# Performance work log

Hardware: AMD Instinct MI355X
Metric: run time of the kernel (lower is better)

The kernel has to match this reference:

```python
import jax, jax.numpy as jnp
import numpy as np

B, W, C = 128, 64, 48
NUM_CHARS, E, H, HM, CTX, CTXM, OUT = 256, 64, 128, 128, 128, 128, 8


def _gru(x, lens, Wih, Whh, bih, bhh):
    """Masked unidirectional GRU. x: [N,T,D], lens: [N]. Outputs zero at t>=len
    (matching pad_packed_sequence), state frozen past len."""
    N, T, _ = x.shape
    Hd = Whh.shape[1]
    xg = jnp.einsum('ntd,gd->ntg', x, Wih) + bih  # [N,T,3H] precomputed input gates

    def step(h, inp):
        xg_t, t = inp
        hg = h @ Whh.T + bhh
        xr, xz, xn = jnp.split(xg_t, 3, axis=-1)
        hr, hz, hn = jnp.split(hg, 3, axis=-1)
        r = jax.nn.sigmoid(xr + hr)
        z = jax.nn.sigmoid(xz + hz)
        n = jnp.tanh(xn + r * hn)
        hnew = (1 - z) * n + z * h
        valid = (t < lens)[:, None]
        h2 = jnp.where(valid, hnew, h)
        out = jnp.where(valid, hnew, jnp.zeros_like(hnew))
        return h2, out

    h0 = jnp.zeros((N, Hd), x.dtype)
    _, outs = jax.lax.scan(step, h0, (xg.transpose(1, 0, 2), jnp.arange(T)))
    return outs.transpose(1, 0, 2)  # [N,T,H]


def _rev(x, lens):
    """Reverse each sequence within its valid length; pad positions unchanged."""
    T = x.shape[1]
    t = jnp.arange(T)[None, :]
    idx = jnp.where(t < lens[:, None], lens[:, None] - 1 - t, t)
    return jnp.take_along_axis(x, idx[:, :, None], axis=1)


def _bigru(x, lens, Wf, Uf, bif, bhf, Wb, Ub, bib, bhb):
    of = _gru(x, lens, Wf, Uf, bif, bhf)
    ob = _rev(_gru(_rev(x, lens), lens, Wb, Ub, bib, bhb), lens)
    return jnp.concatenate([of, ob], axis=-1)


def _attn_pool(out, Wp, bp, ctx):
    # out: [N,T,K]; softmax over ALL T positions (pads have out=0, faithful to source)
    proj = jnp.tanh(jnp.einsum('ntk,ck->ntc', out, Wp) + bp)
    att = jax.nn.softmax(proj @ ctx, axis=1)  # [N,T]
    return jnp.einsum('nt,ntk->nk', att, out)


def setup_inputs():
    key = jax.random.key(0)
    ks = iter(jax.random.split(key, 40))
    nrm = lambda shape: jax.random.normal(next(ks), shape, jnp.float32) * 0.1
    chars = jax.random.randint(next(ks), (B, W, C), 0, NUM_CHARS, dtype=jnp.int32)
    lens = jax.random.randint(next(ks), (B, W), 1, C + 1, dtype=jnp.int32)
    inp = dict(chars=chars, lens=lens, emb=nrm((NUM_CHARS, E)))
    for p, din, h in [('c', E, H), ('m', 2 * H, HM)]:
        for d in ('f', 'b'):
            inp[p + 'Wih_' + d] = nrm((3 * h, din))
            inp[p + 'Whh_' + d] = nrm((3 * h, h))
            inp[p + 'bih_' + d] = nrm((3 * h,))
            inp[p + 'bhh_' + d] = nrm((3 * h,))
    inp.update(wWp=nrm((CTX, 2 * H)), wbp=nrm((CTX,)), wctx=nrm((CTX,)),
               pWp=nrm((CTXM, 2 * HM)), pbp=nrm((CTXM,)), pctx=nrm((CTXM,)),
               Wout=nrm((OUT, 2 * HM)), bout=nrm((OUT,)))
    return inp


def reference(chars, lens, emb,
              cWih_f, cWhh_f, cbih_f, cbhh_f, cWih_b, cWhh_b, cbih_b, cbhh_b,
              mWih_f, mWhh_f, mbih_f, mbhh_f, mWih_b, mWhh_b, mbih_b, mbhh_b,
              wWp, wbp, wctx, pWp, pbp, pctx, Wout, bout):
    Bb, Ww, Cc = chars.shape
    x = emb[chars.reshape(Bb * Ww, Cc)]        # [B*W, C, E]
    l = lens.reshape(Bb * Ww)
    char_out = _bigru(x, l, cWih_f, cWhh_f, cbih_f, cbhh_f,
                      cWih_b, cWhh_b, cbih_b, cbhh_b)  # [B*W, C, 2H]
    words = _attn_pool(char_out, wWp, wbp, wctx).reshape(Bb, Ww, -1)  # [B, W, 2H]
    lw = jnp.full((Bb,), Ww, dtype=lens.dtype)
    msg_out = _bigru(words, lw, mWih_f, mWhh_f, mbih_f, mbhh_f,
                     mWih_b, mWhh_b, mbih_b, mbhh_b)  # [B, W, 2HM]
    messages = _attn_pool(msg_out, pWp, pbp, pctx)     # [B, 2HM]
    outputs = messages @ Wout.T + bout                 # [B, OUT]
    return outputs, messages
```

## Files before the change

### kernel.cpp

```cpp
#include <hip/hip_runtime.h>
#include <stdint.h>
#include <stddef.h>

#define NCH   256
#define EDIM  64
#define HDIM  128
#define G3    384
#define BATCH 128
#define WRD   64
#define CLEN  48
#define NW    8192
#define OUTD  8

#define LOG2E 1.44269504088896f

#define C_EMB     0
#define C_CWIH_F  16384
#define C_CWHH_F  40960
#define C_CBIH_F  90112
#define C_CBHH_F  90496
#define C_CWIH_B  90880
#define C_CWHH_B  115456
#define C_CBIH_B  164608
#define C_CBHH_B  164992
#define C_MWIH_F  165376
#define C_MWHH_F  263680
#define C_MBIH_F  312832
#define C_MBHH_F  313600
#define C_MWIH_B  314368
#define C_MWHH_B  412672
#define C_MBIH_B  461824
#define C_MBHH_B  462592
#define C_WWP     463360
#define C_WBP     496128
#define C_WCTX    496256
#define C_PWP     496384
#define C_PBP     529152
#define C_PCTX    529280
#define C_WOUT    529408
#define C_BOUT    531456
#define C_TOTAL   531464

#define OFF_FLAG    0u
#define OFF_CANON   1024u
#define OFF_WPFRAG  (4u*1024u*1024u)
#define OFF_PFRAG   (4u*1024u*1024u + 65536u)
#define OFF_MFRAG   (4u*1024u*1024u + 131072u)
#define OFF_BIASV   (4u*1024u*1024u + 524288u)
#define OFF_ORD     (4u*1024u*1024u + 532480u)
#define OFF_XGT4    5111808u
#define OFF_WORDS   35651584u
#define OFF_MSGOUT  47185920u
#define OFF_CHOUT   54525952u

typedef _Float16 h2v __attribute__((ext_vector_type(2)));
typedef _Float16 f16x8 __attribute__((ext_vector_type(8)));
typedef float f32x4 __attribute__((ext_vector_type(4)));

__device__ __forceinline__ float bf16_to_f32(unsigned short u){
  union{unsigned int i;float f;}v; v.i=((unsigned int)u)<<16; return v.f;
}
__device__ __forceinline__ unsigned short f32_to_bf16(float f){
  union{float f;unsigned int i;}v; v.f=f;
  unsigned int u=v.i; unsigned int r=(u + 0x7fffu + ((u>>16)&1u))>>16;
  return (unsigned short)r;
}
__device__ __forceinline__ uint32_t pack_h2(float x,float y){
  h2v h; h[0]=(_Float16)x; h[1]=(_Float16)y; uint32_t u; __builtin_memcpy(&u,&h,4); return u;
}
__device__ __forceinline__ unsigned short f32_to_h16u(float f){
  _Float16 h=(_Float16)f; unsigned short u; __builtin_memcpy(&u,&h,2); return u;
}
__device__ __forceinline__ float dot2(uint32_t a, uint32_t b, float c){
#if __has_builtin(__builtin_amdgcn_fdot2)
  h2v av,bv; __builtin_memcpy(&av,&a,4); __builtin_memcpy(&bv,&b,4);
  return __builtin_amdgcn_fdot2(av,bv,c,false);
#else
  h2v av,bv; __builtin_memcpy(&av,&a,4); __builtin_memcpy(&bv,&b,4);
  return c + (float)av[0]*(float)bv[0] + (float)av[1]*(float)bv[1];
#endif
}
__device__ __forceinline__ float exp2_fast(float x){
#if __has_builtin(__builtin_amdgcn_exp2f)
  return __builtin_amdgcn_exp2f(x);
#else
  return exp2f(x);
#endif
}
__device__ __forceinline__ float rcp_fast(float x){
#if __has_builtin(__builtin_amdgcn_rcpf)
  return __builtin_amdgcn_rcpf(x);
#else
  return 1.f/x;
#endif
}
__device__ __forceinline__ float sig2(float s){ return rcp_fast(1.f+exp2_fast(s)); }
__device__ __forceinline__ float tanh2(float u){ return fmaf(-2.f, rcp_fast(exp2_fast(u)+1.f), 1.f); }
__device__ __forceinline__ float wave_sum(float v){
  #pragma unroll
  for(int m=32;m>=1;m>>=1) v += __shfl_xor(v,m,64);
  return v;
}
__device__ __forceinline__ float wave_max(float v){
  #pragma unroll
  for(int m=32;m>=1;m>>=1) v = fmaxf(v,__shfl_xor(v,m,64));
  return v;
}
__device__ __forceinline__ f32x4 mfma16(f16x8 a, f16x8 b, f32x4 c){
  return __builtin_amdgcn_mfma_f32_16x16x32_f16(a, b, c, 0, 0, 0);
}

struct ConvArgs { const void* src[25]; int len[25]; int off[25]; };

__global__ void k_convert(ConvArgs a, int* __restrict__ flag, float* __restrict__ dst){
  const unsigned short* u=(const unsigned short*)a.src[0];
  int found=0;
  for(int i=threadIdx.x;i<2048;i+=256){ float v=bf16_to_f32(u[i]); if(fabsf(v)>8.f) found=1; }
  __shared__ int s;
  if(threadIdx.x==0) s=0;
  __syncthreads();
  if(found) atomicOr(&s,1);
  __syncthreads();
  int isf32=s;
  if(blockIdx.x==0 && threadIdx.x==0) *flag=isf32;
  int idx=blockIdx.x*256+threadIdx.x;
  #pragma unroll 1
  for(int i=0;i<25;i++){
    if(idx < a.len[i]){
      float v = isf32 ? ((const float*)a.src[i])[idx]
                      : bf16_to_f32(((const unsigned short*)a.src[i])[idx]);
      dst[a.off[i]+idx]=v;
      return;
    }
    idx -= a.len[i];
  }
}

__global__ void k_sort(const int* __restrict__ lensp, int* __restrict__ ord){
  __shared__ int hist[64];
  __shared__ int base[64];
  int tid=threadIdx.x;
  if(tid<64) hist[tid]=0;
  __syncthreads();
  for(int i=tid;i<NW;i+=256) atomicAdd(&hist[48-lensp[i]],1);
  __syncthreads();
  if(tid==0){ int s=0; for(int b=0;b<64;b++){ base[b]=s; s+=hist[b]; } }
  __syncthreads();
  for(int i=tid;i<NW;i+=256){
    int b=48-lensp[i];
    int pos=atomicAdd(&base[b],1);
    ord[pos]=i;
  }
}

__global__ void k_prep(const float* __restrict__ cw, unsigned short* __restrict__ wpfrag,
                       unsigned short* __restrict__ pfrag, unsigned short* __restrict__ mfrag,
                       float* __restrict__ biasv){
  int idx=blockIdx.x*256+threadIdx.x;
  if(idx<32768){
    int j=idx&7, lane=(idx>>3)&63, nt=(idx>>9)&7, ks=idx>>12;
    int nl=lane&15, q=lane>>4;
    float v = cw[C_WWP + (nt*16+nl)*256 + ks*32 + q*8 + j] * (2.f*LOG2E);
    wpfrag[idx]=f32_to_h16u(v);
  } else if(idx<65536){
    int i=idx-32768;
    int j=i&7, lane=(i>>3)&63, nt=(i>>9)&7, ks=i>>12;
    int nl=lane&15, q=lane>>4;
    float v = cw[C_PWP + (nt*16+nl)*256 + ks*32 + q*8 + j] * (2.f*LOG2E);
    pfrag[i]=f32_to_h16u(v);
  } else if(idx<262144){
    int i=idx-65536;
    int j=i&7, lane=(i>>3)&63, t2=i>>9;
    int nt=t2%48, ks=t2/48;
    int n=nt*16+(lane&15), k=ks*32+(lane>>4)*8+j;
    int gate = (n<G3)? n : n-G3;
    float sc = (gate<256)? -LOG2E : 2.f*LOG2E;
    float v = ((n<G3)? cw[C_MWIH_F + n*256 + k] : cw[C_MWIH_B + (n-G3)*256 + k]) * sc;
    mfrag[i]=f32_to_h16u(v);
  } else if(idx<262912){
    int i=idx-262144;
    int dir=i/384, g=i-384*(i/384);
    float b = cw[(dir?C_MBIH_B:C_MBIH_F)+g] + ((g<256)? cw[(dir?C_MBHH_B:C_MBHH_F)+g] : 0.f);
    biasv[i] = b * ((g<256)? -LOG2E : 2.f*LOG2E);
  } else if(idx==262912){
    float a=0.f;
    for(int c=0;c<128;c++) a += tanh2(cw[C_WBP+c]*(2.f*LOG2E))*cw[C_WCTX+c];
    biasv[768]=a;
  }
}

__global__ __launch_bounds__(512) void k_prepx(const float* __restrict__ cw,
                                               float4* __restrict__ xgt4){
  int tid=threadIdx.x;
  int w=tid>>6, L=tid&63, nl=L&15, q=L>>4;
  int mchunk=blockIdx.x, dir=blockIdx.y;
  const float* Wih=cw+(dir?C_CWIH_B:C_CWIH_F);
  const float* bih=cw+(dir?C_CBIH_B:C_CBIH_F);
  const float* bhh=cw+(dir?C_CBHH_B:C_CBHH_F);
  int c16=w*16+nl;

  f16x8 bw[3][2];
  #pragma unroll
  for(int i=0;i<3;i++){
    int n=(w+8*i)*16+nl;
    const float* wr=Wih + n*EDIM;
    #pragma unroll
    for(int ks=0;ks<2;ks++){
      const float4* p=(const float4*)(wr + ks*32 + q*8);
      float4 v0=p[0], v1=p[1];
      f16x8 f;
      f[0]=(_Float16)v0.x; f[1]=(_Float16)v0.y; f[2]=(_Float16)v0.z; f[3]=(_Float16)v0.w;
      f[4]=(_Float16)v1.x; f[5]=(_Float16)v1.y; f[6]=(_Float16)v1.z; f[7]=(_Float16)v1.w;
      bw[i][ks]=f;
    }
  }
  float br=bih[c16]+bhh[c16];
  float bz=bih[128+c16]+bhh[128+c16];
  float bn=bih[256+c16];

  #pragma unroll
  for(int mt=0;mt<2;mt++){
    int ch=mchunk*32+mt*16+nl;
    f32x4 ar={0,0,0,0}, az={0,0,0,0}, an={0,0,0,0};
    #pragma unroll
    for(int ks=0;ks<2;ks++){
      const float4* p=(const float4*)(cw + C_EMB + ch*EDIM + ks*32 + q*8);
      float4 v0=p[0], v1=p[1];
      f16x8 a;
      a[0]=(_Float16)v0.x; a[1]=(_Float16)v0.y; a[2]=(_Float16)v0.z; a[3]=(_Float16)v0.w;
      a[4]=(_Float16)v1.x; a[5]=(_Float16)v1.y; a[6]=(_Float16)v1.z; a[7]=(_Float16)v1.w;
      ar=mfma16(a,bw[0][ks],ar); az=mfma16(a,bw[1][ks],az); an=mfma16(a,bw[2][ks],an);
    }
    #pragma unroll
    for(int r=0;r<4;r++){
      int chr=mchunk*32+mt*16+q*4+r;
      xgt4[dir*32768 + chr*128 + c16] =
        make_float4((ar[r]+br)*(-LOG2E), (az[r]+bz)*(-LOG2E), (an[r]+bn)*(2.f*LOG2E), 0.f);
    }
  }
}

__global__ __launch_bounds__(512,4) void k_chargru(const int* __restrict__ chars,
    const int* __restrict__ lensp, const int* __restrict__ ord,
    const float* __restrict__ cw, const float4* __restrict__ xgt4,
    unsigned short* __restrict__ chout){
  int tid=threadIdx.x;
  int w=tid>>6, L=tid&63, nl=L&15, q=L>>4;
  int dir=blockIdx.y;
  int seq0=blockIdx.x*16;
  const float* Whh=cw+(dir?C_CWHH_B:C_CWHH_F);
  const float* bhh=cw+(dir?C_CBHH_B:C_CBHH_F);
  const float4* xg4 = xgt4 + (dir<<15);

  int c16=w*16+nl;
  f16x8 bh[3][4];
  const float wsc[3]={-LOG2E,-LOG2E,2.f*LOG2E};
  #pragma unroll
  for(int i=0;i<3;i++){
    int n=(w+8*i)*16+nl;
    const float* wr=Whh + n*HDIM;
    float sc=wsc[i];
    #pragma unroll
    for(int c=0;c<4;c++){
      const float4* p=(const float4*)(wr + c*32 + q*8);
      float4 v0=p[0], v1=p[1];
      f16x8 f;
      f[0]=(_Float16)(v0.x*sc); f[1]=(_Float16)(v0.y*sc); f[2]=(_Float16)(v0.z*sc); f[3]=(_Float16)(v0.w*sc);
      f[4]=(_Float16)(v1.x*sc); f[5]=(_Float16)(v1.y*sc); f[6]=(_Float16)(v1.z*sc); f[7]=(_Float16)(v1.w*sc);
      bh[i][c]=f;
    }
  }
  float bias_hn=bhh[256+c16]*(2.f*LOG2E);

  __shared__ int sord[16];
  __shared__ int cidT[CLEN][16];
  __shared__ int lenS[16];
  __shared__ __align__(16) _Float16 hbuf[2][16][136];

  if(tid<16) sord[tid]=ord[seq0+tid];
  __syncthreads();
  for(int i=tid;i<16*CLEN;i+=512){ int t=i>>4, s=i&15; cidT[t][s]=chars[sord[s]*CLEN+t]; }
  if(tid<16) lenS[tid]=lensp[sord[tid]];
  for(int i=tid;i<16*136/2;i+=512) ((uint32_t*)&hbuf[0][0][0])[i]=0u;
  __syncthreads();

  int maxlen=1;
  #pragma unroll 1
  for(int s=0;s<16;s++) maxlen=max(maxlen,lenS[s]);
  int lenq[4];
  #pragma unroll
  for(int r=0;r<4;r++) lenq[r]=lenS[q*4+r];
  int sw=tid>>5, aw=tid&31;
  int lenp=lenS[sw];
  int sq=sord[sw];

  float4 pf[4];
  {
    int t0 = dir ? maxlen-1 : 0;
    int4 c4=*(const int4*)&cidT[t0][q*4];
    pf[0]=xg4[c4.x*128+c16]; pf[1]=xg4[c4.y*128+c16];
    pf[2]=xg4[c4.z*128+c16]; pf[3]=xg4[c4.w*128+c16];
  }
  float hreg[4]={0.f,0.f,0.f,0.f};
  unsigned short* wp = chout + ((size_t)sq*CLEN + (dir?maxlen-1:0))*256 + dir*HDIM + 4*aw;
  int dstep = dir ? -256 : 256;

  for(int step=0; step<maxlen; ++step){
    int t = dir ? maxlen-1-step : step;
    int p = step&1;
    float4 qf[4];
    bool havepf = (step+1 < maxlen);
    if(havepf){
      int tn = dir ? maxlen-2-step : step+1;
      int4 c4=*(const int4*)&cidT[tn][q*4];
      qf[0]=xg4[c4.x*128+c16]; qf[1]=xg4[c4.y*128+c16];
      qf[2]=xg4[c4.z*128+c16]; qf[3]=xg4[c4.w*128+c16];
    }
    f32x4 ra={0,0,0,0}, rb={0,0,0,0}, za={0,0,0,0}, zb={0,0,0,0};
    f32x4 ha={bias_hn,bias_hn,bias_hn,bias_hn}, hb={0,0,0,0};
    const _Float16* hrow=&hbuf[p][nl][0];
    f16x8 af0=*(const f16x8*)(hrow + 0*32 + q*8);
    f16x8 af1=*(const f16x8*)(hrow + 1*32 + q*8);
    f16x8 af2=*(const f16x8*)(hrow + 2*32 + q*8);
    f16x8 af3=*(const f16x8*)(hrow + 3*32 + q*8);
    ra=mfma16(af0,bh[0][0],ra); za=mfma16(af0,bh[1][0],za); ha=mfma16(af0,bh[2][0],ha);
    rb=mfma16(af1,bh[0][1],rb); zb=mfma16(af1,bh[1][1],zb); hb=mfma16(af1,bh[2][1],hb);
    ra=mfma16(af2,bh[0][2],ra); za=mfma16(af2,bh[1][2],za); ha=mfma16(af2,bh[2][2],ha);
    rb=mfma16(af3,bh[0][3],rb); zb=mfma16(af3,bh[1][3],zb); hb=mfma16(af3,bh[2][3],hb);
    f32x4 accr=ra+rb, accz=za+zb, a2h=ha+hb;
    #pragma unroll
    for(int r=0;r<4;r++){
      float rg=sig2(accr[r]+pf[r].x);
      float zg=sig2(accz[r]+pf[r].y);
      float nn=tanh2(fmaf(rg,a2h[r],pf[r].z));
      float hnew=fmaf(zg,hreg[r]-nn,nn);
      bool valid = t < lenq[r];
      float hv = valid ? hnew : hreg[r];
      hreg[r]=hv;
      hbuf[p^1][q*4+r][c16]=(_Float16)hv;
    }
    __syncthreads();
    if(t<lenp){
      uint2 d=*(const uint2*)&hbuf[p^1][sw][4*aw];
      *(uint2*)wp = d;
    }
    wp += dstep;
    if(havepf){
      #pragma unroll
      for(int r=0;r<4;r++) pf[r]=qf[r];
    }
  }
}

__global__ __launch_bounds__(256,4) void k_wpool(const unsigned short* __restrict__ chout,
    const unsigned short* __restrict__ wpfrag, const float* __restrict__ bp,
    const float* __restrict__ ctxv, const int* __restrict__ lensp,
    const float* __restrict__ L0p, _Float16* __restrict__ wordsF16){
  int n=blockIdx.x, tid=threadIdx.x;
  int w=tid>>6, lane=tid&63, nl=lane&15, q=lane>>4;
  int len=lensp[n];
  float L0=*L0p;
  __shared__ __align__(16) _Float16 sa[48][264];
  __shared__ float redl[48][4];
  __shared__ float att[48];

  uint4 bfr[2][8];
  const uint4* wp4=(const uint4*)wpfrag;
  #pragma unroll
  for(int ks=0;ks<8;ks++){
    bfr[0][ks]=wp4[(ks*8+2*w  )*64+lane];
    bfr[1][ks]=wp4[(ks*8+2*w+1)*64+lane];
  }
  {
    const uint4* src=(const uint4*)(chout + (size_t)n*48*256);
    #pragma unroll 1
    for(int ii=tid; ii<len*32; ii+=256){
      int row=ii>>5, c16=ii&31;
      *(uint4*)&sa[row][c16*8]=src[ii];
    }
  }
  __syncthreads();

  int mtmax=(len+15)>>4;
  f32x4 acc[3][2];
  #pragma unroll
  for(int mt=0;mt<3;mt++){ acc[mt][0]=(f32x4){0,0,0,0}; acc[mt][1]=(f32x4){0,0,0,0}; }
  #pragma unroll
  for(int ks=0;ks<8;ks++){
    f16x8 b0,b1;
    __builtin_memcpy(&b0,&bfr[0][ks],16);
    __builtin_memcpy(&b1,&bfr[1][ks],16);
    #pragma unroll
    for(int mt=0;mt<3;mt++){
      if(mt<mtmax){
        f16x8 af=*(const f16x8*)&sa[mt*16+nl][ks*32+q*8];
        acc[mt][0]=mfma16(af,b0,acc[mt][0]);
        acc[mt][1]=mfma16(af,b1,acc[mt][1]);
      }
    }
  }
  int c0=(2*w)*16+nl, c1=c0+16;
  float bp0=bp[c0]*(2.f*LOG2E), bp1=bp[c1]*(2.f*LOG2E);
  float cv0=ctxv[c0], cv1=ctxv[c1];
  #pragma unroll
  for(int mt=0;mt<3;mt++){
    if(mt<mtmax){
      #pragma unroll
      for(int r=0;r<4;r++){
        float v=tanh2(acc[mt][0][r]+bp0)*cv0 + tanh2(acc[mt][1][r]+bp1)*cv1;
        v+=__shfl_xor(v,1,64); v+=__shfl_xor(v,2,64);
        v+=__shfl_xor(v,4,64); v+=__shfl_xor(v,8,64);
        if(nl==0) redl[mt*16+q*4+r][w]=v;
      }
    }
  }
  __syncthreads();
  if(tid<64){
    float v;
    if(tid<len) v=redl[tid][0]+redl[tid][1]+redl[tid][2]+redl[tid][3];
    else if(tid<48) v=L0;
    else v=-1e30f;
    float mx=wave_max(v);
    float e=(tid<48)?exp2_fast((v-mx)*LOG2E):0.f;
    float s=wave_sum(e);
    if(tid<48) att[tid]=e*rcp_fast(s);
  }
  __syncthreads();
  float a=0.f;
  #pragma unroll 1
  for(int t=0;t<len;t++) a=fmaf(att[t],(float)sa[t][tid],a);
  wordsF16[(size_t)n*256+tid]=(_Float16)a;
}

__global__ __launch_bounds__(384) void k_msggru(const float* __restrict__ cw,
    const _Float16* __restrict__ wordsF16, const unsigned short* __restrict__ mfrag,
    const float* __restrict__ biasv, unsigned short* __restrict__ msg_out){
  int dir=blockIdx.y, b=blockIdx.x, tid=threadIdx.x;
  int w=tid>>6, lane=tid&63, nl=lane&15, q=lane>>4;

  __shared__ _Float16 xgL[64][392];
  __shared__ __align__(16) _Float16 hh[HDIM];
  __shared__ float rr[HDIM], zz[HDIM], xns[HDIM], hns[HDIM];

  {
    int ntb = dir*24 + w*4;
    const uint4* mf4=(const uint4*)mfrag;
    const uint4* wv=(const uint4*)wordsF16;
    f32x4 acc[4][4];
    #pragma unroll
    for(int mt=0;mt<4;mt++)
      #pragma unroll
      for(int i=0;i<4;i++) acc[mt][i]=(f32x4){0,0,0,0};
    #pragma unroll
    for(int ks=0;ks<8;ks++){
      f16x8 bf[4];
      #pragma unroll
      for(int i=0;i<4;i++){
        uint4 u=mf4[((ks*48 + ntb+i)*64 + lane)];
        __builtin_memcpy(&bf[i],&u,16);
      }
      #pragma unroll
      for(int mt=0;mt<4;mt++){
        uint4 u=wv[((size_t)b*64 + mt*16 + nl)*32 + ks*4 + q];
        f16x8 av; __builtin_memcpy(&av,&u,16);
        #pragma unroll
        for(int i=0;i<4;i++) acc[mt][i]=mfma16(av,bf[i],acc[mt][i]);
      }
    }
    float bi[4];
    #pragma unroll
    for(int i=0;i<4;i++) bi[i]=biasv[dir*384 + (w*4+i)*16+nl];
    #pragma unroll
    for(int mt=0;mt<4;mt++)
      #pragma unroll
      for(int i=0;i<4;i++){
        int g=(w*4+i)*16+nl;
        #pragma unroll
        for(int r=0;r<4;r++)
          xgL[mt*16+q*4+r][g]=(_Float16)(acc[mt][i][r]+bi[i]);
      }
  }

  const float* Whh=cw+(dir?C_MWHH_B:C_MWHH_F);
  const float* bhh=cw+(dir?C_MBHH_B:C_MBHH_F);
  uint32_t whh[64];
  {
    float sc = (tid<256) ? -LOG2E : 2.f*LOG2E;
    const float4* h4=(const float4*)(Whh + tid*HDIM);
    #pragma unroll
    for(int i=0;i<32;i++){ float4 v=h4[i]; whh[2*i]=pack_h2(v.x*sc,v.y*sc); whh[2*i+1]=pack_h2(v.z*sc,v.w*sc); }
  }
  float ha0 = (tid>=256) ? bhh[tid]*(2.f*LOG2E) : 0.f;
  if(tid<64) ((uint32_t*)hh)[tid]=0u;
  float hreg=0.f;
  __syncthreads();
  int j=tid&127, gt=tid>>7;
  for(int step=0;step<WRD;step++){
    int wt = dir ? (WRD-1-step) : step;
    float xacc = (float)xgL[wt][tid];
    float ha=ha0;
    const uint4* hp=(const uint4*)hh;
    #pragma unroll
    for(int qq=0;qq<16;qq++){ uint4 v=hp[qq];
      ha=dot2(whh[4*qq+0],v.x,ha); ha=dot2(whh[4*qq+1],v.y,ha);
      ha=dot2(whh[4*qq+2],v.z,ha); ha=dot2(whh[4*qq+3],v.w,ha); }
    if(gt==0)      rr[j]=sig2(xacc+ha);
    else if(gt==1) zz[j]=sig2(xacc+ha);
    else { xns[j]=xacc; hns[j]=ha; }
    __syncthreads();
    if(tid<HDIM){
      float r=rr[tid], z=zz[tid];
      float nn=tanh2(fmaf(r,hns[tid],xns[tid]));
      float hnew=fmaf(z,hreg-nn,nn);
      hreg=hnew;
      hh[tid]=(_Float16)hnew;
      msg_out[(size_t)(b*WRD+wt)*256 + dir*HDIM + tid]=f32_to_h16u(hnew);
    }
    __syncthreads();
  }
}

__global__ __launch_bounds__(256) void k_mpool(const unsigned short* __restrict__ outp,
    const unsigned short* __restrict__ pfrag, const float* __restrict__ bp,
    const float* __restrict__ ctxv,
    const float* __restrict__ Wout, const float* __restrict__ bout,
    void* dout, const int* __restrict__ flag){
  int n=blockIdx.x, tid=threadIdx.x;
  int w=tid>>6, lane=tid&63, nl=lane&15, q=lane>>4;
  __shared__ __align__(16) _Float16 sa[64][264];
  __shared__ float redl[64][4];
  __shared__ float att[64];
  __shared__ float msgv[256];

  uint4 bfr[2][8];
  const uint4* pf4=(const uint4*)pfrag;
  #pragma unroll
  for(int ks=0;ks<8;ks++){
    bfr[0][ks]=pf4[(ks*8+2*w  )*64+lane];
    bfr[1][ks]=pf4[(ks*8+2*w+1)*64+lane];
  }
  {
    const uint4* src=(const uint4*)(outp + (size_t)n*64*256);
    #pragma unroll
    for(int i=0;i<8;i++){
      int ii=tid+256*i; int row=ii>>5, c16=ii&31;
      *(uint4*)&sa[row][c16*8]=src[ii];
    }
  }
  __syncthreads();

  f32x4 acc[4][2];
  #pragma unroll
  for(int mt=0;mt<4;mt++){ acc[mt][0]=(f32x4){0,0,0,0}; acc[mt][1]=(f32x4){0,0,0,0}; }
  #pragma unroll
  for(int ks=0;ks<8;ks++){
    f16x8 b0,b1;
    __builtin_memcpy(&b0,&bfr[0][ks],16);
    __builtin_memcpy(&b1,&bfr[1][ks],16);
    #pragma unroll
    for(int mt=0;mt<4;mt++){
      f16x8 af=*(const f16x8*)&sa[mt*16+nl][ks*32+q*8];
      acc[mt][0]=mfma16(af,b0,acc[mt][0]);
      acc[mt][1]=mfma16(af,b1,acc[mt][1]);
    }
  }
  int c0=(2*w)*16+nl, c1=c0+16;
  float bp0=bp[c0]*(2.f*LOG2E), bp1=bp[c1]*(2.f*LOG2E);
  float cv0=ctxv[c0], cv1=ctxv[c1];
  #pragma unroll
  for(int mt=0;mt<4;mt++){
    #pragma unroll
    for(int r=0;r<4;r++){
      float v=tanh2(acc[mt][0][r]+bp0)*cv0 + tanh2(acc[mt][1][r]+bp1)*cv1;
      v+=__shfl_xor(v,1,64); v+=__shfl_xor(v,2,64);
      v+=__shfl_xor(v,4,64); v+=__shfl_xor(v,8,64);
      if(nl==0) redl[mt*16+q*4+r][w]=v;
    }
  }
  __syncthreads();
  if(tid<64){
    float v=redl[tid][0]+redl[tid][1]+redl[tid][2]+redl[tid][3];
    float mx=wave_max(v);
    float e=exp2_fast((v-mx)*LOG2E);
    float s=wave_sum(e);
    att[tid]=e*rcp_fast(s);
  }
  __syncthreads();
  float a=0.f;
  #pragma unroll 1
  for(int t=0;t<64;t++) a=fmaf(att[t],(float)sa[t][tid],a);
  msgv[tid]=a;
  if(*flag){ ((float*)dout)[1024 + n*256 + tid]=a; }
  else { ((unsigned short*)dout)[1024 + n*256 + tid]=f32_to_bf16(a); }
  __syncthreads();
  if(tid<OUTD){
    float acc2=bout[tid];
    #pragma unroll 1
    for(int k=0;k<256;k++) acc2=fmaf(msgv[k], Wout[tid*256+k], acc2);
    if(*flag) ((float*)dout)[n*OUTD+tid]=acc2;
    else ((unsigned short*)dout)[n*OUTD+tid]=f32_to_bf16(acc2);
  }
}

extern "C" void kernel_launch(void* const* d_in, const int* in_sizes, int n_in,
                              void* d_out, int out_size, void* d_ws, size_t ws_size,
                              hipStream_t stream){
  (void)in_sizes; (void)n_in; (void)out_size; (void)ws_size;
  char* ws=(char*)d_ws;
  int* flag=(int*)(ws+OFF_FLAG);
  float* canon=(float*)(ws+OFF_CANON);
  unsigned short* wpfrag=(unsigned short*)(ws+OFF_WPFRAG);
  unsigned short* pfrag=(unsigned short*)(ws+OFF_PFRAG);
  unsigned short* mfrag=(unsigned short*)(ws+OFF_MFRAG);
  float* biasv=(float*)(ws+OFF_BIASV);
  int* ord=(int*)(ws+OFF_ORD);
  float4* xgt4=(float4*)(ws+OFF_XGT4);
  _Float16* wordsF16=(_Float16*)(ws+OFF_WORDS);
  unsigned short* msgout=(unsigned short*)(ws+OFF_MSGOUT);
  unsigned short* chout=(unsigned short*)(ws+OFF_CHOUT);
  const int* chars=(const int*)d_in[0];
  const int* lensp=(const int*)d_in[1];

  ConvArgs ca;
  static const int clen_[25]={16384,24576,49152,384,384,24576,49152,384,384,
                              98304,49152,768,768,98304,49152,768,768,
                              32768,128,128,32768,128,128,2048,8};
  int off=0;
  for(int i=0;i<25;i++){ ca.src[i]=d_in[i+2]; ca.len[i]=clen_[i]; ca.off[i]=off; off+=clen_[i]; }
  hipLaunchKernelGGL(k_convert, dim3((C_TOTAL+255)/256), dim3(256), 0, stream, ca, flag, canon);
  hipLaunchKernelGGL(k_sort, dim3(1), dim3(256), 0, stream, lensp, ord);
  hipLaunchKernelGGL(k_prep, dim3(1028), dim3(256), 0, stream, canon, wpfrag, pfrag, mfrag, biasv);
  hipLaunchKernelGGL(k_prepx, dim3(8,2), dim3(512), 0, stream, canon, xgt4);
  hipLaunchKernelGGL(k_chargru, dim3(NW/16,2), dim3(512), 0, stream, chars, lensp, ord, canon, xgt4, chout);
  hipLaunchKernelGGL(k_wpool, dim3(NW), dim3(256), 0, stream, chout, wpfrag,
                     canon+C_WBP, canon+C_WCTX, lensp, biasv+768, wordsF16);
  hipLaunchKernelGGL(k_msggru, dim3(BATCH,2), dim3(384), 0, stream, canon, wordsF16, mfrag, biasv, msgout);
  hipLaunchKernelGGL(k_mpool, dim3(BATCH), dim3(256), 0, stream, msgout, pfrag,
                     canon+C_PBP, canon+C_PCTX,
                     canon+C_WOUT, canon+C_BOUT, d_out, flag);
}
```

Before: 506.8 us.

## Fuse char BiGRU directions and word attention pooling into one kernel

Merges the character GRU and the word attention-pool kernels into a single kernel. Each block now runs the forward direction and then the backward direction one after the other, instead of using separate blocks per direction. During the backward pass it computes the attention scores and keeps a running (online) softmax weighted sum, reading the stored forward outputs back step by step. This drops the k_wpool launch and the full 256-wide character-output round trip through memory. The cost is half as many blocks, a serial dependency chain twice as long per block, and extra barriers in every backward step.

```diff
diff --git a/kernel.cpp b/kernel.cpp
--- a/kernel.cpp
+++ b/kernel.cpp
@@ -240,48 +240,30 @@
   }
 }
 
-__global__ __launch_bounds__(512,4) void k_chargru(const int* __restrict__ chars,
+__global__ __launch_bounds__(512,4) void k_char(const int* __restrict__ chars,
     const int* __restrict__ lensp, const int* __restrict__ ord,
     const float* __restrict__ cw, const float4* __restrict__ xgt4,
-    unsigned short* __restrict__ chout){
+    const unsigned short* __restrict__ wpfrag, const float* __restrict__ bp,
+    const float* __restrict__ ctxv, const float* __restrict__ L0p,
+    _Float16* __restrict__ chout, _Float16* __restrict__ wordsF16){
   int tid=threadIdx.x;
   int w=tid>>6, L=tid&63, nl=L&15, q=L>>4;
-  int dir=blockIdx.y;
   int seq0=blockIdx.x*16;
-  const float* Whh=cw+(dir?C_CWHH_B:C_CWHH_F);
-  const float* bhh=cw+(dir?C_CBHH_B:C_CBHH_F);
-  const float4* xg4 = xgt4 + (dir<<15);
-
   int c16=w*16+nl;
-  f16x8 bh[3][4];
-  const float wsc[3]={-LOG2E,-LOG2E,2.f*LOG2E};
-  #pragma unroll
-  for(int i=0;i<3;i++){
-    int n=(w+8*i)*16+nl;
-    const float* wr=Whh + n*HDIM;
-    float sc=wsc[i];
-    #pragma unroll
-    for(int c=0;c<4;c++){
-      const float4* p=(const float4*)(wr + c*32 + q*8);
-      float4 v0=p[0], v1=p[1];
-      f16x8 f;
-      f[0]=(_Float16)(v0.x*sc); f[1]=(_Float16)(v0.y*sc); f[2]=(_Float16)(v0.z*sc); f[3]=(_Float16)(v0.w*sc);
-      f[4]=(_Float16)(v1.x*sc); f[5]=(_Float16)(v1.y*sc); f[6]=(_Float16)(v1.z*sc); f[7]=(_Float16)(v1.w*sc);
-      bh[i][c]=f;
-    }
-  }
-  float bias_hn=bhh[256+c16]*(2.f*LOG2E);
-
-  __shared__ int sord[16];
+
+  __shared__ int sordS[16];
+  __shared__ int lenS[16];
   __shared__ int cidT[CLEN][16];
-  __shared__ int lenS[16];
   __shared__ __align__(16) _Float16 hbuf[2][16][136];
-
-  if(tid<16) sord[tid]=ord[seq0+tid];
-  __syncthreads();
-  for(int i=tid;i<16*CLEN;i+=512){ int t=i>>4, s=i&15; cidT[t][s]=chars[sord[s]*CLEN+t]; }
-  if(tid<16) lenS[tid]=lensp[sord[tid]];
-  for(int i=tid;i<16*136/2;i+=512) ((uint32_t*)&hbuf[0][0][0])[i]=0u;
+  __shared__ __align__(16) _Float16 obuf[16][264];
+  __shared__ float Nacc[16][264];
+  __shared__ float redl[16][8];
+  __shared__ float mS[16], dS[16], aS[16], eS[16];
+
+  if(tid<16) sordS[tid]=ord[seq0+tid];
+  __syncthreads();
+  if(tid<16) lenS[tid]=lensp[sordS[tid]];
+  for(int i=tid;i<16*CLEN;i+=512){ int t=i>>4, s=i&15; cidT[t][s]=chars[sordS[s]*CLEN+t]; }
   __syncthreads();
 
   int maxlen=1;
@@ -292,144 +274,164 @@
   for(int r=0;r<4;r++) lenq[r]=lenS[q*4+r];
   int sw=tid>>5, aw=tid&31;
   int lenp=lenS[sw];
-  int sq=sord[sw];
-
-  float4 pf[4];
+  size_t sqbase=(size_t)sordS[sw]*48*128;
+  float bpw=bp[c16]*(2.f*LOG2E), cvw=ctxv[c16];
+  float L0=*L0p;
+
+  #pragma unroll 1
+  for(int dir=0; dir<2; ++dir){
+    const float* Whh=cw+(dir?C_CWHH_B:C_CWHH_F);
+    const float* bhh=cw+(dir?C_CBHH_B:C_CBHH_F);
+    const float4* xg4 = xgt4 + (dir<<15);
+    f16x8 bh[3][4];
+    const float wsc0 = -LOG2E, wsc2 = 2.f*LOG2E;
+    #pragma unroll
+    for(int i=0;i<3;i++){
+      int n=(w+8*i)*16+nl;
+      const float* wr=Whh + n*HDIM;
+      float sc = (i==2)? wsc2 : wsc0;
+      #pragma unroll
+      for(int c=0;c<4;c++){
+        const float4* p=(const float4*)(wr + c*32 + q*8);
+        float4 v0=p[0], v1=p[1];
+        f16x8 f;
+        f[0]=(_Float16)(v0.x*sc); f[1]=(_Float16)(v0.y*sc); f[2]=(_Float16)(v0.z*sc); f[3]=(_Float16)(v0.w*sc);
+        f[4]=(_Float16)(v1.x*sc); f[5]=(_Float16)(v1.y*sc); f[6]=(_Float16)(v1.z*sc); f[7]=(_Float16)(v1.w*sc);
+        bh[i][c]=f;
+      }
+    }
+    float bias_hn=bhh[256+c16]*(2.f*LOG2E);
+    f16x8 wfr[8];
+    if(dir){
+      const uint4* wp4=(const uint4*)wpfrag;
+      #pragma unroll
+      for(int ks=0;ks<8;ks++){
+        uint4 u=wp4[(ks*8+w)*64+L];
+        __builtin_memcpy(&wfr[ks],&u,16);
+      }
+    }
+    __syncthreads();
+    for(int i=tid;i<16*136;i+=512){ ((uint32_t*)&hbuf[0][0][0])[i&0xffff]=0u; }
+    for(int i=tid;i<2176;i+=512) ((uint32_t*)&hbuf[0][0][0])[i]=0u;
+    if(dir){
+      for(int i=tid;i<16*264;i+=512) ((float*)&Nacc[0][0])[i]=0.f;
+      if(tid<16){ mS[tid]=-1e30f; dS[tid]=0.f; }
+    }
+    float hreg[4]={0.f,0.f,0.f,0.f};
+    __syncthreads();
+
+    float4 pf[4];
+    {
+      int t0 = dir ? maxlen-1 : 0;
+      int4 c4=*(const int4*)&cidT[t0][q*4];
+      pf[0]=xg4[c4.x*128+c16]; pf[1]=xg4[c4.y*128+c16];
+      pf[2]=xg4[c4.z*128+c16]; pf[3]=xg4[c4.w*128+c16];
+    }
+    _Float16* wpo = chout + sqbase + 4*aw;
+
+    #pragma unroll 1
+    for(int step=0; step<maxlen; ++step){
+      int t = dir ? maxlen-1-step : step;
+      int p = step&1;
+      float4 qf[4];
+      bool havepf = (step+1 < maxlen);
+      if(havepf){
+        int tn = dir ? maxlen-2-step : step+1;
+        int4 c4=*(const int4*)&cidT[tn][q*4];
+        qf[0]=xg4[c4.x*128+c16]; qf[1]=xg4[c4.y*128+c16];
+        qf[2]=xg4[c4.z*128+c16]; qf[3]=xg4[c4.w*128+c16];
+      }
+      if(dir && tid<256){
+        int s=tid>>4, u=tid&15;
+        uint4 v=make_uint4(0,0,0,0);
+        if(t<lenS[s]) v=((const uint4*)(chout + ((size_t)sordS[s]*48+t)*128))[u];
+        *(uint4*)&obuf[s][u*8]=v;
+      }
+      f32x4 ra={0,0,0,0}, rb={0,0,0,0}, za={0,0,0,0}, zb={0,0,0,0};
+      f32x4 ha={bias_hn,bias_hn,bias_hn,bias_hn}, hb={0,0,0,0};
+      const _Float16* hrow=&hbuf[p][nl][0];
+      f16x8 af0=*(const f16x8*)(hrow + 0*32 + q*8);
+      f16x8 af1=*(const f16x8*)(hrow + 1*32 + q*8);
+      f16x8 af2=*(const f16x8*)(hrow + 2*32 + q*8);
+      f16x8 af3=*(const f16x8*)(hrow + 3*32 + q*8);
+      ra=mfma16(af0,bh[0][0],ra); za=mfma16(af0,bh[1][0],za); ha=mfma16(af0,bh[2][0],ha);
+      rb=mfma16(af1,bh[0][1],rb); zb=mfma16(af1,bh[1][1],zb); hb=mfma16(af1,bh[2][1],hb);
+      ra=mfma16(af2,bh[0][2],ra); za=mfma16(af2,bh[1][2],za); ha=mfma16(af2,bh[2][2],ha);
+      rb=mfma16(af3,bh[0][3],rb); zb=mfma16(af3,bh[1][3],zb); hb=mfma16(af3,bh[2][3],hb);
+      f32x4 accr=ra+rb, accz=za+zb, a2h=ha+hb;
+      #pragma unroll
+      for(int r=0;r<4;r++){
+        float rg=sig2(accr[r]+pf[r].x);
+        float zg=sig2(accz[r]+pf[r].y);
+        float nn=tanh2(fmaf(rg,a2h[r],pf[r].z));
+        float hnew=fmaf(zg,hreg[r]-nn,nn);
+        bool valid = t < lenq[r];
+        float hv = valid ? hnew : hreg[r];
+        hreg[r]=hv;
+        hbuf[p^1][q*4+r][c16]=(_Float16)hv;
+        if(dir) obuf[q*4+r][128+c16] = valid ? (_Float16)hnew : (_Float16)0.f;
+      }
+      __syncthreads();
+      if(!dir){
+        if(t<lenp){
+          uint2 d=*(const uint2*)&hbuf[p^1][sw][4*aw];
+          *(uint2*)(wpo + (size_t)t*128) = d;
+        }
+      } else {
+        f32x4 pa={0,0,0,0};
+        #pragma unroll
+        for(int ks=0;ks<8;ks++){
+          f16x8 af=*(const f16x8*)&obuf[nl][ks*32+q*8];
+          pa=mfma16(af,wfr[ks],pa);
+        }
+        #pragma unroll
+        for(int r=0;r<4;r++){
+          float v=tanh2(pa[r]+bpw)*cvw;
+          v+=__shfl_xor(v,1,64); v+=__shfl_xor(v,2,64);
+          v+=__shfl_xor(v,4,64); v+=__shfl_xor(v,8,64);
+          if(nl==0) redl[q*4+r][w]=v;
+        }
+        __syncthreads();
+        if(tid<16){
+          float l=redl[tid][0]+redl[tid][1]+redl[tid][2]+redl[tid][3]
+                 +redl[tid][4]+redl[tid][5]+redl[tid][6]+redl[tid][7];
+          float m0=mS[tid];
+          float m1=fmaxf(m0,l);
+          float al=exp2_fast((m0-m1)*LOG2E);
+          float e =exp2_fast((l -m1)*LOG2E);
+          dS[tid]=dS[tid]*al+e; mS[tid]=m1; aS[tid]=al; eS[tid]=e;
+        }
+        __syncthreads();
+        {
+          int s=tid>>5; int cc=(tid&31)*8;
+          float al=aS[s], e=eS[s];
+          f16x8 ov=*(const f16x8*)&obuf[s][cc];
+          #pragma unroll
+          for(int k2=0;k2<8;k2++) Nacc[s][cc+k2]=fmaf(Nacc[s][cc+k2],al,e*(float)ov[k2]);
+        }
+        __syncthreads();
+      }
+      #pragma unroll
+      for(int r=0;r<4;r++) pf[r]=qf[r];
+    }
+  }
+  if(tid<16){
+    float m0=mS[tid];
+    float m1=fmaxf(m0,L0);
+    float al=exp2_fast((m0-m1)*LOG2E);
+    float d=dS[tid]*al + (float)(48-maxlen)*exp2_fast((L0-m1)*LOG2E);
+    aS[tid]=al*rcp_fast(d);
+  }
+  __syncthreads();
   {
-    int t0 = dir ? maxlen-1 : 0;
-    int4 c4=*(const int4*)&cidT[t0][q*4];
-    pf[0]=xg4[c4.x*128+c16]; pf[1]=xg4[c4.y*128+c16];
-    pf[2]=xg4[c4.z*128+c16]; pf[3]=xg4[c4.w*128+c16];
-  }
-  float hreg[4]={0.f,0.f,0.f,0.f};
-  unsigned short* wp = chout + ((size_t)sq*CLEN + (dir?maxlen-1:0))*256 + dir*HDIM + 4*aw;
-  int dstep = dir ? -256 : 256;
-
-  for(int step=0; step<maxlen; ++step){
-    int t = dir ? maxlen-1-step : step;
-    int p = step&1;
-    float4 qf[4];
-    bool havepf = (step+1 < maxlen);
-    if(havepf){
-      int tn = dir ? maxlen-2-step : step+1;
-      int4 c4=*(const int4*)&cidT[tn][q*4];
-      qf[0]=xg4[c4.x*128+c16]; qf[1]=xg4[c4.y*128+c16];
-      qf[2]=xg4[c4.z*128+c16]; qf[3]=xg4[c4.w*128+c16];
-    }
-    f32x4 ra={0,0,0,0}, rb={0,0,0,0}, za={0,0,0,0}, zb={0,0,0,0};
-    f32x4 ha={bias_hn,bias_hn,bias_hn,bias_hn}, hb={0,0,0,0};
-    const _Float16* hrow=&hbuf[p][nl][0];
-    f16x8 af0=*(const f16x8*)(hrow + 0*32 + q*8);
-    f16x8 af1=*(const f16x8*)(hrow + 1*32 + q*8);
-    f16x8 af2=*(const f16x8*)(hrow + 2*32 + q*8);
-    f16x8 af3=*(const f16x8*)(hrow + 3*32 + q*8);
-    ra=mfma16(af0,bh[0][0],ra); za=mfma16(af0,bh[1][0],za); ha=mfma16(af0,bh[2][0],ha);
-    rb=mfma16(af1,bh[0][1],rb); zb=mfma16(af1,bh[1][1],zb); hb=mfma16(af1,bh[2][1],hb);
-    ra=mfma16(af2,bh[0][2],ra); za=mfma16(af2,bh[1][2],za); ha=mfma16(af2,bh[2][2],ha);
-    rb=mfma16(af3,bh[0][3],rb); zb=mfma16(af3,bh[1][3],zb); hb=mfma16(af3,bh[2][3],hb);
-    f32x4 accr=ra+rb, accz=za+zb, a2h=ha+hb;
-    #pragma unroll
-    for(int r=0;r<4;r++){
-      float rg=sig2(accr[r]+pf[r].x);
-      float zg=sig2(accz[r]+pf[r].y);
-      float nn=tanh2(fmaf(rg,a2h[r],pf[r].z));
-      float hnew=fmaf(zg,hreg[r]-nn,nn);
-      bool valid = t < lenq[r];
-      float hv = valid ? hnew : hreg[r];
-      hreg[r]=hv;
-      hbuf[p^1][q*4+r][c16]=(_Float16)hv;
-    }
-    __syncthreads();
-    if(t<lenp){
-      uint2 d=*(const uint2*)&hbuf[p^1][sw][4*aw];
-      *(uint2*)wp = d;
-    }
-    wp += dstep;
-    if(havepf){
-      #pragma unroll
-      for(int r=0;r<4;r++) pf[r]=qf[r];
-    }
-  }
-}
-
-__global__ __launch_bounds__(256,4) void k_wpool(const unsigned short* __restrict__ chout,
-    const unsigned short* __restrict__ wpfrag, const float* __restrict__ bp,
-    const float* __restrict__ ctxv, const int* __restrict__ lensp,
-    const float* __restrict__ L0p, _Float16* __restrict__ wordsF16){
-  int n=blockIdx.x, tid=threadIdx.x;
-  int w=tid>>6, lane=tid&63, nl=lane&15, q=lane>>4;
-  int len=lensp[n];
-  float L0=*L0p;
-  __shared__ __align__(16) _Float16 sa[48][264];
-  __shared__ float redl[48][4];
-  __shared__ float att[48];
-
-  uint4 bfr[2][8];
-  const uint4* wp4=(const uint4*)wpfrag;
-  #pragma unroll
-  for(int ks=0;ks<8;ks++){
-    bfr[0][ks]=wp4[(ks*8+2*w  )*64+lane];
-    bfr[1][ks]=wp4[(ks*8+2*w+1)*64+lane];
-  }
-  {
-    const uint4* src=(const uint4*)(chout + (size_t)n*48*256);
-    #pragma unroll 1
-    for(int ii=tid; ii<len*32; ii+=256){
-      int row=ii>>5, c16=ii&31;
-      *(uint4*)&sa[row][c16*8]=src[ii];
-    }
-  }
-  __syncthreads();
-
-  int mtmax=(len+15)>>4;
-  f32x4 acc[3][2];
-  #pragma unroll
-  for(int mt=0;mt<3;mt++){ acc[mt][0]=(f32x4){0,0,0,0}; acc[mt][1]=(f32x4){0,0,0,0}; }
-  #pragma unroll
-  for(int ks=0;ks<8;ks++){
-    f16x8 b0,b1;
-    __builtin_memcpy(&b0,&bfr[0][ks],16);
-    __builtin_memcpy(&b1,&bfr[1][ks],16);
-    #pragma unroll
-    for(int mt=0;mt<3;mt++){
-      if(mt<mtmax){
-        f16x8 af=*(const f16x8*)&sa[mt*16+nl][ks*32+q*8];
-        acc[mt][0]=mfma16(af,b0,acc[mt][0]);
-        acc[mt][1]=mfma16(af,b1,acc[mt][1]);
-      }
-    }
-  }
-  int c0=(2*w)*16+nl, c1=c0+16;
-  float bp0=bp[c0]*(2.f*LOG2E), bp1=bp[c1]*(2.f*LOG2E);
-  float cv0=ctxv[c0], cv1=ctxv[c1];
-  #pragma unroll
-  for(int mt=0;mt<3;mt++){
-    if(mt<mtmax){
-      #pragma unroll
-      for(int r=0;r<4;r++){
-        float v=tanh2(acc[mt][0][r]+bp0)*cv0 + tanh2(acc[mt][1][r]+bp1)*cv1;
-        v+=__shfl_xor(v,1,64); v+=__shfl_xor(v,2,64);
-        v+=__shfl_xor(v,4,64); v+=__shfl_xor(v,8,64);
-        if(nl==0) redl[mt*16+q*4+r][w]=v;
-      }
-    }
-  }
-  __syncthreads();
-  if(tid<64){
-    float v;
-    if(tid<len) v=redl[tid][0]+redl[tid][1]+redl[tid][2]+redl[tid][3];
-    else if(tid<48) v=L0;
-    else v=-1e30f;
-    float mx=wave_max(v);
-    float e=(tid<48)?exp2_fast((v-mx)*LOG2E):0.f;
-    float s=wave_sum(e);
-    if(tid<48) att[tid]=e*rcp_fast(s);
-  }
-  __syncthreads();
-  float a=0.f;
-  #pragma unroll 1
-  for(int t=0;t<len;t++) a=fmaf(att[t],(float)sa[t][tid],a);
-  wordsF16[(size_t)n*256+tid]=(_Float16)a;
+    int s=tid>>5; int cc=(tid&31)*8;
+    float sc=aS[s];
+    f16x8 o;
+    #pragma unroll
+    for(int k2=0;k2<8;k2++) o[k2]=(_Float16)(Nacc[s][cc+k2]*sc);
+    uint4 u; __builtin_memcpy(&u,&o,16);
+    *(uint4*)&wordsF16[(size_t)sordS[s]*256+cc]=u;
+  }
 }
 
 __global__ __launch_bounds__(384) void k_msggru(const float* __restrict__ cw,
@@ -617,7 +619,7 @@
   float4* xgt4=(float4*)(ws+OFF_XGT4);
   _Float16* wordsF16=(_Float16*)(ws+OFF_WORDS);
   unsigned short* msgout=(unsigned short*)(ws+OFF_MSGOUT);
-  unsigned short* chout=(unsigned short*)(ws+OFF_CHOUT);
+  _Float16* chout=(_Float16*)(ws+OFF_CHOUT);
   const int* chars=(const int*)d_in[0];
   const int* lensp=(const int*)d_in[1];
 
@@ -631,9 +633,9 @@
   hipLaunchKernelGGL(k_sort, dim3(1), dim3(256), 0, stream, lensp, ord);
   hipLaunchKernelGGL(k_prep, dim3(1028), dim3(256), 0, stream, canon, wpfrag, pfrag, mfrag, biasv);
   hipLaunchKernelGGL(k_prepx, dim3(8,2), dim3(512), 0, stream, canon, xgt4);
-  hipLaunchKernelGGL(k_chargru, dim3(NW/16,2), dim3(512), 0, stream, chars, lensp, ord, canon, xgt4, chout);
-  hipLaunchKernelGGL(k_wpool, dim3(NW), dim3(256), 0, stream, chout, wpfrag,
-                     canon+C_WBP, canon+C_WCTX, lensp, biasv+768, wordsF16);
+  hipLaunchKernelGGL(k_char, dim3(NW/16), dim3(512), 0, stream, chars, lensp, ord,
+                     canon, xgt4, wpfrag, canon+C_WBP, canon+C_WCTX, biasv+768,
+                     chout, wordsF16);
   hipLaunchKernelGGL(k_msggru, dim3(BATCH,2), dim3(384), 0, stream, canon, wordsF16, mfrag, biasv, msgout);
   hipLaunchKernelGGL(k_mpool, dim3(BATCH), dim3(256), 0, stream, msgout, pfrag,
                      canon+C_PBP, canon+C_PCTX,
```

Result: slower. 825.8 us (+62.9%).
